# Performance work log

Measured on AMD Instinct MI355X. Metric: run time of the kernel, lower is better.

The kernel has to match this reference:

```python
import jax, jax.numpy as jnp
import numpy as np

B, C, H, W = 32, 512, 56, 56
P = 64  # planes = C / ratio
EPS = 1e-3


def setup_inputs() -> dict:
    key = jax.random.key(0)
    ks = jax.random.split(key, 10)
    return {
        "x": jax.random.normal(ks[0], (B, C, H, W), jnp.float32),
        "wm": jax.random.normal(ks[1], (1, C), jnp.float32) * 0.05,
        "bm": jax.random.normal(ks[2], (1,), jnp.float32) * 0.05,
        "w1": jax.random.normal(ks[3], (P, C), jnp.float32) * 0.05,
        "b1": jax.random.normal(ks[4], (P,), jnp.float32) * 0.05,
        "ln_g": jax.random.normal(ks[5], (P,), jnp.float32) * 0.1 + 1.0,
        "ln_b": jax.random.normal(ks[6], (P,), jnp.float32) * 0.05,
        "w2": jax.random.normal(ks[7], (C, P), jnp.float32) * 0.05,
        "b2": jax.random.normal(ks[8], (C,), jnp.float32) * 0.05,
        "gamma": jax.random.normal(ks[9], (1,), jnp.float32) * 0.1,
    }


def reference(x, wm, bm, w1, b1, ln_g, ln_b, w2, b2, gamma):
    b, c, h, w = x.shape
    xf = x.reshape(b, c, h * w)                       # (B, C, S)
    # attention spatial pool: 1x1 conv mask -> softmax over spatial -> weighted sum
    mask = jnp.einsum('bcs,c->bs', xf, wm[0]) + bm[0]  # (B, S)
    attn = jax.nn.softmax(mask, axis=-1)               # softmax over H*W
    context = jnp.einsum('bcs,bs->bc', xf, attn)       # (B, C)
    # channel_add_conv: 1x1 conv -> LayerNorm([P,1,1], eps=1e-3) -> ReLU -> 1x1 conv
    hid = jnp.einsum('pc,bc->bp', w1, context) + b1    # (B, P)
    mu = hid.mean(axis=-1, keepdims=True)
    var = jnp.mean((hid - mu) ** 2, axis=-1, keepdims=True)
    hid = (hid - mu) / jnp.sqrt(var + EPS) * ln_g + ln_b
    hid = jax.nn.relu(hid)
    add = jnp.einsum('cp,bp->bc', w2, hid) + b2        # (B, C)
    return x + gamma[0] * add[:, :, None, None]
```

## Files before the change

kernel.cpp:

```cpp
#include <hip/hip_runtime.h>

constexpr int kB = 32;
constexpr int kC = 512;
constexpr int kS = 56 * 56;
constexpr int kP = 64;
constexpr float kEps = 1e-3f;

constexpr int kSG = 32;
constexpr int kNG = kS / kSG;
constexpr int kCW = kC / 2;
static_assert(kS % kSG == 0, "group must divide S");

typedef float f4v __attribute__((ext_vector_type(4)));

__global__ __launch_bounds__(128, 2)
void k_pass_a(const float* __restrict__ x, const float* __restrict__ wm,
              float* __restrict__ pc, float* __restrict__ pmz) {
    __shared__ float swm[kC];
    __shared__ f4v   pmw[2][8];

    const int t  = threadIdx.x;
    const int w  = t >> 6;
    const int l  = t & 63;
    const int si = l & 7;
    const int cg = l >> 3;
    const int b  = blockIdx.y;
    const int g  = blockIdx.x;
    const int s0 = g * kSG;

    swm[t]       = wm[t];
    swm[t + 128] = wm[t + 128];
    swm[t + 256] = wm[t + 256];
    swm[t + 384] = wm[t + 384];

    const float* xb = x + (size_t)b * kC * kS
                        + (size_t)(w * kCW + cg) * kS + s0 + si * 4;

    f4v xt[32];
#pragma unroll
    for (int k = 0; k < 32; ++k)
        xt[k] = *(const f4v*)(xb + (size_t)(8 * k) * kS);

    __syncthreads();

    float m0 = 0.f, m1 = 0.f, m2 = 0.f, m3 = 0.f;
#pragma unroll
    for (int k = 0; k < 32; ++k) {
        const float wv = swm[w * kCW + cg + 8 * k];
        m0 += xt[k].x * wv; m1 += xt[k].y * wv;
        m2 += xt[k].z * wv; m3 += xt[k].w * wv;
    }

#pragma unroll
    for (int k = 0; k < 32; ++k) asm volatile("" : "+v"(xt[k]));

#pragma unroll
    for (int off = 8; off <= 32; off <<= 1) {
        m0 += __shfl_xor(m0, off); m1 += __shfl_xor(m1, off);
        m2 += __shfl_xor(m2, off); m3 += __shfl_xor(m3, off);
    }

    if (l < 8) pmw[w][si] = (f4v){m0, m1, m2, m3};
    __syncthreads();
    {
        const f4v o = pmw[w ^ 1][si];
        m0 += o.x; m1 += o.y; m2 += o.z; m3 += o.w;
    }

    float mm = fmaxf(fmaxf(m0, m1), fmaxf(m2, m3));
    mm = fmaxf(mm, __shfl_xor(mm, 1));
    mm = fmaxf(mm, __shfl_xor(mm, 2));
    mm = fmaxf(mm, __shfl_xor(mm, 4));
    const float e0 = expf(m0 - mm), e1 = expf(m1 - mm);
    const float e2 = expf(m2 - mm), e3 = expf(m3 - mm);
    float z = e0 + e1 + e2 + e3;
    z += __shfl_xor(z, 1); z += __shfl_xor(z, 2); z += __shfl_xor(z, 4);
    if (t == 0) {
        pmz[(b * kNG + g) * 2 + 0] = mm;
        pmz[(b * kNG + g) * 2 + 1] = z;
    }

    float* pco = pc + ((size_t)b * kNG + g) * kC + w * kCW;
#pragma unroll
    for (int k = 0; k < 32; ++k) {
        float p = xt[k].x * e0 + xt[k].y * e1 + xt[k].z * e2 + xt[k].w * e3;
        p += __shfl_xor(p, 1); p += __shfl_xor(p, 2); p += __shfl_xor(p, 4);
        if (si == 0) pco[8 * k + cg] = p;
    }
}

__global__ __launch_bounds__(512)
void k_combine_mlp(const float* __restrict__ pc, const float* __restrict__ pmz,
                   const float* __restrict__ w1, const float* __restrict__ b1,
                   const float* __restrict__ ln_g, const float* __restrict__ ln_b,
                   const float* __restrict__ w2, const float* __restrict__ b2,
                   const float* __restrict__ gamma, float* __restrict__ add) {
    const int b = blockIdx.x;
    const int t = threadIdx.x;
    __shared__ float scale[kNG];
    __shared__ float ctx[kC];
    __shared__ float hp[kP][9];
    __shared__ float hid[kP];

    if (t < 64) {
        const float m1 = (t      < kNG) ? pmz[(b * kNG + t     ) * 2] : -INFINITY;
        const float m2 = (t + 64 < kNG) ? pmz[(b * kNG + t + 64) * 2] : -INFINITY;
        float m = fmaxf(m1, m2);
        for (int off = 32; off; off >>= 1) m = fmaxf(m, __shfl_xor(m, off));
        const float e1 = (t      < kNG) ? expf(m1 - m) : 0.f;
        const float e2 = (t + 64 < kNG) ? expf(m2 - m) : 0.f;
        float z = 0.f;
        if (t      < kNG) z += pmz[(b * kNG + t     ) * 2 + 1] * e1;
        if (t + 64 < kNG) z += pmz[(b * kNG + t + 64) * 2 + 1] * e2;
        for (int off = 32; off; off >>= 1) z += __shfl_xor(z, off);
        const float inv = 1.f / z;
        if (t      < kNG) scale[t]      = e1 * inv;
        if (t + 64 < kNG) scale[t + 64] = e2 * inv;
    }
    __syncthreads();

    {
        float acc = 0.f;
        for (int i = 0; i < kNG; ++i)
            acc += pc[((size_t)b * kNG + i) * kC + t] * scale[i];
        ctx[t] = acc;
    }
    __syncthreads();

    {
        const int p = t & 63, k = t >> 6;
        const float* w1p = w1 + p * kC + k * 64;
        const float* cxp = ctx + k * 64;
        float acc = 0.f;
#pragma unroll 8
        for (int i = 0; i < 64; ++i) acc += w1p[i] * cxp[i];
        hp[p][k] = acc;
    }
    __syncthreads();

    if (t < 64) {
        float h = b1[t];
#pragma unroll
        for (int k = 0; k < 8; ++k) h += hp[t][k];
        float mu = h;
        for (int off = 32; off; off >>= 1) mu += __shfl_xor(mu, off);
        mu *= (1.f / kP);
        const float d = h - mu;
        float var = d * d;
        for (int off = 32; off; off >>= 1) var += __shfl_xor(var, off);
        var *= (1.f / kP);
        const float hv = d * rsqrtf(var + kEps) * ln_g[t] + ln_b[t];
        hid[t] = fmaxf(hv, 0.f);
    }
    __syncthreads();

    {
        float a = b2[t];
        const float* w2c = w2 + t * kP;
#pragma unroll
        for (int p = 0; p < kP; ++p) a += w2c[p] * hid[p];
        add[b * kC + t] = gamma[0] * a;
    }
}

constexpr int kOutBlocks = (kB * kC * kS / 4) / (256 * 16);
static_assert(kOutBlocks * 256 * 16 == kB * kC * kS / 4, "exact tiling");

__global__ __launch_bounds__(256)
void k_out(const float* __restrict__ x, const float* __restrict__ addv,
           float* __restrict__ out) {
    const size_t base = (size_t)blockIdx.x * 4096 + threadIdx.x;
#pragma unroll
    for (int j = 0; j < 16; ++j) {
        const size_t i4 = base + (size_t)j * 256;
        const float a = addv[i4 / (kS / 4)];
        const f4v xv = ((const f4v*)x)[i4];
        const f4v o = {xv.x + a, xv.y + a, xv.z + a, xv.w + a};
        ((f4v*)out)[i4] = o;
    }
}

extern "C" void kernel_launch(void* const* d_in, const int* in_sizes, int n_in,
                              void* d_out, int out_size, void* d_ws, size_t ws_size,
                              hipStream_t stream) {
    const float* x     = (const float*)d_in[0];
    const float* wm    = (const float*)d_in[1];
    const float* w1    = (const float*)d_in[3];
    const float* b1    = (const float*)d_in[4];
    const float* ln_g  = (const float*)d_in[5];
    const float* ln_b  = (const float*)d_in[6];
    const float* w2    = (const float*)d_in[7];
    const float* b2    = (const float*)d_in[8];
    const float* gamma = (const float*)d_in[9];
    float* out = (float*)d_out;

    float* ws  = (float*)d_ws;
    float* pc  = ws;
    float* pmz = pc + (size_t)kB * kNG * kC;
    float* add = pmz + (size_t)kB * kNG * 2;

    k_pass_a<<<dim3(kNG, kB), 128, 0, stream>>>(x, wm, pc, pmz);
    k_combine_mlp<<<kB, 512, 0, stream>>>(pc, pmz, w1, b1, ln_g, ln_b,
                                          w2, b2, gamma, add);
    k_out<<<kOutBlocks, 256, 0, stream>>>(x, add, out);
}
```

Before: 413.9 us.

## Widen pass-A blocks to 512 threads and flatten output kernel with nontemporal stores

The pass-A kernel now uses 512 threads per block, each holding 8 channel vectors instead of 32. This cuts register pressure and raises occupancy, and the softmax partials are combined through shared memory by one wave. The output kernel now handles one float4 per thread with a nontemporal store, so the write stream does not pollute the cache. The cost is more blocks and more sync overhead in pass A, plus a much larger grid for the output kernel.

```diff
diff --git a/kernel.cpp b/kernel.cpp
--- a/kernel.cpp
+++ b/kernel.cpp
@@ -8,84 +8,86 @@
 
 constexpr int kSG = 32;
 constexpr int kNG = kS / kSG;
-constexpr int kCW = kC / 2;
 static_assert(kS % kSG == 0, "group must divide S");
 
 typedef float f4v __attribute__((ext_vector_type(4)));
 
-__global__ __launch_bounds__(128, 2)
+__global__ __launch_bounds__(512)
 void k_pass_a(const float* __restrict__ x, const float* __restrict__ wm,
               float* __restrict__ pc, float* __restrict__ pmz) {
     __shared__ float swm[kC];
-    __shared__ f4v   pmw[2][8];
+    __shared__ f4v   pmw[8][8];
+    __shared__ f4v   es4[kSG / 4];
 
     const int t  = threadIdx.x;
     const int w  = t >> 6;
     const int l  = t & 63;
-    const int si = l & 7;
-    const int cg = l >> 3;
+    const int si = t & 7;
+    const int c0 = t >> 3;
     const int b  = blockIdx.y;
     const int g  = blockIdx.x;
     const int s0 = g * kSG;
 
-    swm[t]       = wm[t];
-    swm[t + 128] = wm[t + 128];
-    swm[t + 256] = wm[t + 256];
-    swm[t + 384] = wm[t + 384];
-
-    const float* xb = x + (size_t)b * kC * kS
-                        + (size_t)(w * kCW + cg) * kS + s0 + si * 4;
-
-    f4v xt[32];
-#pragma unroll
-    for (int k = 0; k < 32; ++k)
-        xt[k] = *(const f4v*)(xb + (size_t)(8 * k) * kS);
+    swm[t] = wm[t];
+
+    const float* xb = x + (size_t)b * kC * kS + (size_t)c0 * kS + s0 + si * 4;
+
+    f4v xt[8];
+#pragma unroll
+    for (int j = 0; j < 8; ++j)
+        xt[j] = *(const f4v*)(xb + (size_t)(64 * j) * kS);
 
     __syncthreads();
 
     float m0 = 0.f, m1 = 0.f, m2 = 0.f, m3 = 0.f;
 #pragma unroll
-    for (int k = 0; k < 32; ++k) {
-        const float wv = swm[w * kCW + cg + 8 * k];
-        m0 += xt[k].x * wv; m1 += xt[k].y * wv;
-        m2 += xt[k].z * wv; m3 += xt[k].w * wv;
-    }
-
-#pragma unroll
-    for (int k = 0; k < 32; ++k) asm volatile("" : "+v"(xt[k]));
+    for (int j = 0; j < 8; ++j) {
+        const float wv = swm[c0 + 64 * j];
+        m0 += xt[j].x * wv; m1 += xt[j].y * wv;
+        m2 += xt[j].z * wv; m3 += xt[j].w * wv;
+    }
+
+#pragma unroll
+    for (int j = 0; j < 8; ++j) asm volatile("" : "+v"(xt[j]));
 
 #pragma unroll
     for (int off = 8; off <= 32; off <<= 1) {
         m0 += __shfl_xor(m0, off); m1 += __shfl_xor(m1, off);
         m2 += __shfl_xor(m2, off); m3 += __shfl_xor(m3, off);
     }
-
     if (l < 8) pmw[w][si] = (f4v){m0, m1, m2, m3};
     __syncthreads();
-    {
-        const f4v o = pmw[w ^ 1][si];
-        m0 += o.x; m1 += o.y; m2 += o.z; m3 += o.w;
-    }
-
-    float mm = fmaxf(fmaxf(m0, m1), fmaxf(m2, m3));
-    mm = fmaxf(mm, __shfl_xor(mm, 1));
-    mm = fmaxf(mm, __shfl_xor(mm, 2));
-    mm = fmaxf(mm, __shfl_xor(mm, 4));
-    const float e0 = expf(m0 - mm), e1 = expf(m1 - mm);
-    const float e2 = expf(m2 - mm), e3 = expf(m3 - mm);
-    float z = e0 + e1 + e2 + e3;
-    z += __shfl_xor(z, 1); z += __shfl_xor(z, 2); z += __shfl_xor(z, 4);
-    if (t == 0) {
-        pmz[(b * kNG + g) * 2 + 0] = mm;
-        pmz[(b * kNG + g) * 2 + 1] = z;
-    }
-
-    float* pco = pc + ((size_t)b * kNG + g) * kC + w * kCW;
-#pragma unroll
-    for (int k = 0; k < 32; ++k) {
-        float p = xt[k].x * e0 + xt[k].y * e1 + xt[k].z * e2 + xt[k].w * e3;
+
+    if (w == 0) {
+        f4v mv = pmw[0][si];
+#pragma unroll
+        for (int ww = 1; ww < 8; ++ww) {
+            const f4v o = pmw[ww][si];
+            mv.x += o.x; mv.y += o.y; mv.z += o.z; mv.w += o.w;
+        }
+        float mm = fmaxf(fmaxf(mv.x, mv.y), fmaxf(mv.z, mv.w));
+        mm = fmaxf(mm, __shfl_xor(mm, 1));
+        mm = fmaxf(mm, __shfl_xor(mm, 2));
+        mm = fmaxf(mm, __shfl_xor(mm, 4));
+        const f4v e = {expf(mv.x - mm), expf(mv.y - mm),
+                       expf(mv.z - mm), expf(mv.w - mm)};
+        float z = e.x + e.y + e.z + e.w;
+        z += __shfl_xor(z, 1); z += __shfl_xor(z, 2); z += __shfl_xor(z, 4);
+        if (l < 8) es4[si] = e;
+        if (l == 0) {
+            pmz[(b * kNG + g) * 2 + 0] = mm;
+            pmz[(b * kNG + g) * 2 + 1] = z;
+        }
+    }
+    __syncthreads();
+
+    const f4v e4 = es4[si];
+    float* pco = pc + ((size_t)b * kNG + g) * kC;
+#pragma unroll
+    for (int j = 0; j < 8; ++j) {
+        float p = xt[j].x * e4.x + xt[j].y * e4.y + xt[j].z * e4.z + xt[j].w * e4.w;
         p += __shfl_xor(p, 1); p += __shfl_xor(p, 2); p += __shfl_xor(p, 4);
-        if (si == 0) pco[8 * k + cg] = p;
+        if (si == 0) pco[c0 + 64 * j] = p;
     }
 }
 
@@ -163,21 +165,18 @@
     }
 }
 
-constexpr int kOutBlocks = (kB * kC * kS / 4) / (256 * 16);
-static_assert(kOutBlocks * 256 * 16 == kB * kC * kS / 4, "exact tiling");
+constexpr unsigned kN4 = (unsigned)((size_t)kB * kC * kS / 4);
+static_assert((size_t)kN4 * 4 == (size_t)kB * kC * kS, "exact");
+static_assert(kN4 % 256 == 0, "exact grid");
 
 __global__ __launch_bounds__(256)
 void k_out(const float* __restrict__ x, const float* __restrict__ addv,
            float* __restrict__ out) {
-    const size_t base = (size_t)blockIdx.x * 4096 + threadIdx.x;
-#pragma unroll
-    for (int j = 0; j < 16; ++j) {
-        const size_t i4 = base + (size_t)j * 256;
-        const float a = addv[i4 / (kS / 4)];
-        const f4v xv = ((const f4v*)x)[i4];
-        const f4v o = {xv.x + a, xv.y + a, xv.z + a, xv.w + a};
-        ((f4v*)out)[i4] = o;
-    }
+    const unsigned i4 = blockIdx.x * 256u + threadIdx.x;
+    const float a = addv[i4 / (kS / 4)];
+    const f4v xv = ((const f4v*)x)[i4];
+    const f4v o = {xv.x + a, xv.y + a, xv.z + a, xv.w + a};
+    __builtin_nontemporal_store(o, (f4v*)out + i4);
 }
 
 extern "C" void kernel_launch(void* const* d_in, const int* in_sizes, int n_in,
@@ -199,8 +198,8 @@
     float* pmz = pc + (size_t)kB * kNG * kC;
     float* add = pmz + (size_t)kB * kNG * 2;
 
-    k_pass_a<<<dim3(kNG, kB), 128, 0, stream>>>(x, wm, pc, pmz);
+    k_pass_a<<<dim3(kNG, kB), 512, 0, stream>>>(x, wm, pc, pmz);
     k_combine_mlp<<<kB, 512, 0, stream>>>(pc, pmz, w1, b1, ln_g, ln_b,
                                           w2, b2, gamma, add);
-    k_out<<<kOutBlocks, 256, 0, stream>>>(x, add, out);
-}
+    k_out<<<kN4 / 256, 256, 0, stream>>>(x, add, out);
+}
```

Result: faster. 396.5 us (-4.2%).
